# Optimization experiments

Measured on AMD Instinct MI355X. Metric: run time of the kernel, lower is better.

## Reference

```python
import jax, jax.numpy as jnp
import numpy as np

B, L, D, H = 8, 1024, 512, 8  # L must equal len_ for the skew trick
DH = D // H


def setup_inputs() -> dict:
    key = jax.random.key(0)
    ks = jax.random.split(key, 6)
    s = 0.02
    return {
        "x": jax.random.normal(ks[0], (B, L, D), dtype=jnp.float32),
        "Wq": jax.random.normal(ks[1], (D, D), dtype=jnp.float32) * s,
        "Wk": jax.random.normal(ks[2], (D, D), dtype=jnp.float32) * s,
        "Wv": jax.random.normal(ks[3], (D, D), dtype=jnp.float32) * s,
        "We": jax.random.normal(ks[4], (L, DH), dtype=jnp.float32) * s,  # e_projection weight: (len_, d_head)
        "Wo": jax.random.normal(ks[5], (D, D), dtype=jnp.float32) * s,
        "bo": jnp.zeros((D,), dtype=jnp.float32),
        "unused": 0,
    }


def reference(x, Wq, Wk, Wv, We, Wo, bo, unused):
    Bx, Lx, Dx = x.shape
    q = (x @ Wq.T).reshape(Bx, Lx, H, DH)  # blhd
    k = (x @ Wk.T).reshape(Bx, Lx, H, DH)
    v = (x @ Wv.T).reshape(Bx, Lx, H, DH)

    # relative-position logits: e_projection(q) then permute -> (B, H, L, len_)
    qe = jnp.einsum('blhd,ed->bhle', q, We)

    # 'skew' trick: reflect-pad right by L-1, zero-pad (right 1, bottom L-1),
    # reshape (B,H,2L-1,2L) -> (B,H,2L,2L-1), slice [:L, L-1:] -> (B,H,L,L)
    qe = jnp.pad(qe, ((0, 0), (0, 0), (0, 0), (0, Lx - 1)), mode='reflect')
    qe = jnp.pad(qe, ((0, 0), (0, 0), (0, Lx - 1), (0, 1)))
    qe = qe.reshape(Bx, H, 2 * Lx, 2 * Lx - 1)
    s_rel = qe[:, :, :Lx, Lx - 1:]

    scale = 1.0 / jnp.sqrt(jnp.asarray(DH, dtype=x.dtype))
    scores = jnp.einsum('blhd,bshd->bhls', q, k)
    A = jax.nn.softmax(scale * (scores + s_rel), axis=-1)
    V = jnp.einsum('bhls,bshd->blhd', A, v).reshape(Bx, Lx, Dx)
    return V @ Wo.T + bo
```

## Files before the change

### kernel.cpp

```cpp
#include <hip/hip_runtime.h>

#define Lc 1024
#define Dc 512
#define Hc 8
#define DHc 64

typedef __attribute__((ext_vector_type(8))) short bf16x8;
typedef __attribute__((ext_vector_type(4))) float f32x4;

typedef __attribute__((address_space(1))) const unsigned int guint;
typedef __attribute__((address_space(3))) unsigned int luint;

__device__ __forceinline__ void gload_lds16(const void* g, void* l) {
    __builtin_amdgcn_global_load_lds((guint*)g, (luint*)l, 16, 0, 0);
}

__device__ __forceinline__ unsigned short f2bf(float f) {
    unsigned u = __float_as_uint(f);
    u += 0x7fffu + ((u >> 16) & 1u);
    return (unsigned short)(u >> 16);
}
__device__ __forceinline__ unsigned short f2bft(float f) {
    return (unsigned short)(__float_as_uint(f) >> 16);
}
__device__ __forceinline__ unsigned pk2(float a, float b) {
    return (unsigned)f2bf(a) | ((unsigned)f2bf(b) << 16);
}
__device__ __forceinline__ float bf2f(unsigned short s) { return __uint_as_float(((unsigned)s) << 16); }

__global__ void cvt_all_kernel(
    const float* __restrict__ x,  const float* __restrict__ Wq,
    const float* __restrict__ Wk, const float* __restrict__ Wv,
    const float* __restrict__ Wo, const float* __restrict__ We,
    unsigned short* __restrict__ xb,  unsigned short* __restrict__ wqb,
    unsigned short* __restrict__ wkb, unsigned short* __restrict__ wvb,
    unsigned short* __restrict__ wob, unsigned short* __restrict__ wet)
{
    int bid = blockIdx.x;
    const float* src; unsigned short* dst; size_t base;
    if      (bid < 4096) { src = x;  dst = xb;  base = (size_t)bid * 1024; }
    else if (bid < 4352) { src = Wq; dst = wqb; base = (size_t)(bid-4096) * 1024; }
    else if (bid < 4608) { src = Wk; dst = wkb; base = (size_t)(bid-4352) * 1024; }
    else if (bid < 4864) { src = Wv; dst = wvb; base = (size_t)(bid-4608) * 1024; }
    else if (bid < 5120) { src = Wo; dst = wob; base = (size_t)(bid-4864) * 1024; }
    else                 { src = We; dst = wet; base = (size_t)(bid-5120) * 1024; }
    size_t i = base + (size_t)threadIdx.x * 4;
    float4 a = *(const float4*)&src[i];
    *(uint2*)&dst[i] = make_uint2(pk2(a.x, a.y), pk2(a.z, a.w));
}

__global__ __launch_bounds__(256, 3) void proj_mfma_kernel(
    const unsigned short* __restrict__ xb,
    const unsigned short* __restrict__ wq, const unsigned short* __restrict__ wk,
    const unsigned short* __restrict__ wv,
    unsigned short* __restrict__ qo, unsigned short* __restrict__ ko,
    unsigned short* __restrict__ vtg, float qscale)
{
    const unsigned short* W;
    if (blockIdx.z == 0)      W = wq;
    else if (blockIdx.z == 1) W = wk;
    else                      W = wv;

    __shared__ unsigned short smem[128 * 136];
    unsigned short* As = smem;
    unsigned short* Bs = smem + 8192;

    const int t = threadIdx.x;
    const int lane = t & 63, w = t >> 6;
    const int lq = lane >> 4, ln = lane & 15;
    const int m0 = blockIdx.y * 128, n0 = blockIdx.x * 128;
    const int wm = (w & 1) * 64, wn = (w >> 1) * 64;
    const int srow = t >> 3;
    const int lsg  = ((t & 7) ^ ((t >> 3) & 7)) * 8;
    const int key  = ln & 7;

    f32x4 acc[4][4];
    #pragma unroll
    for (int i = 0; i < 4; i++)
        #pragma unroll
        for (int j = 0; j < 4; j++) acc[i][j] = (f32x4){0.f,0.f,0.f,0.f};

    for (int c0 = 0; c0 < 512; c0 += 64) {
        __syncthreads();
        #pragma unroll
        for (int g = 0; g < 4; g++) {
            gload_lds16(&xb[(size_t)(m0 + 32*g + srow) * 512 + c0 + lsg], &As[(32*g + srow)*64 + (t&7)*8]);
            gload_lds16(&W [(size_t)(n0 + 32*g + srow) * 512 + c0 + lsg], &Bs[(32*g + srow)*64 + (t&7)*8]);
        }
        __syncthreads();

        #pragma unroll
        for (int kk = 0; kk < 2; kk++) {
            bf16x8 af[4], bf[4];
            #pragma unroll
            for (int i = 0; i < 4; i++)
                af[i] = *(bf16x8*)&As[(wm + 16*i + ln)*64 + ((kk*4 + lq) ^ key)*8];
            #pragma unroll
            for (int j = 0; j < 4; j++)
                bf[j] = *(bf16x8*)&Bs[(wn + 16*j + ln)*64 + ((kk*4 + lq) ^ key)*8];
            #pragma unroll
            for (int i = 0; i < 4; i++)
                #pragma unroll
                for (int j = 0; j < 4; j++)
                    acc[i][j] = __builtin_amdgcn_mfma_f32_16x16x32_bf16(af[i], bf[j], acc[i][j], 0, 0, 0);
        }
    }

    if (blockIdx.z < 2) {
        unsigned short* out = (blockIdx.z == 0) ? qo : ko;
        const float osc = (blockIdx.z == 0) ? qscale : 1.0f;
        #pragma unroll
        for (int i = 0; i < 4; i++) {
            #pragma unroll
            for (int r = 0; r < 4; r++) {
                int m = m0 + wm + 16*i + 4*lq + r;
                int b = m >> 10, l = m & 1023;
                #pragma unroll
                for (int j = 0; j < 4; j++) {
                    int n = n0 + wn + 16*j + ln;
                    int h = n >> 6, dh = n & 63;
                    out[((size_t)((b*Hc + h)*Lc + l))*DHc + dh] = f2bf(acc[i][j][r] * osc);
                }
            }
        }
    } else {
        __syncthreads();
        unsigned short* Ts = smem;
        #pragma unroll
        for (int i = 0; i < 4; i++) {
            int mlb = wm + 16*i + 4*lq;
            #pragma unroll
            for (int j = 0; j < 4; j++) {
                int nl = wn + 16*j + ln;
                *(uint2*)&Ts[nl*136 + mlb] = make_uint2(pk2(acc[i][j][0], acc[i][j][1]),
                                                        pk2(acc[i][j][2], acc[i][j][3]));
            }
        }
        __syncthreads();
        const int b = m0 >> 10, l0m = m0 & 1023;
        const int nl = t >> 1, seg = (t & 1) * 64;
        const int ng = n0 + nl, h = ng >> 6, dh = ng & 63;
        unsigned short* dst = vtg + (((size_t)(b*Hc + h))*DHc + dh)*Lc + l0m + seg;
        #pragma unroll
        for (int u = 0; u < 8; u++)
            *(uint4*)&dst[8*u] = *(uint4*)&Ts[nl*136 + seg + 8*u];
    }
}

__global__ __launch_bounds__(256, 4) void out_mfma_kernel(
    const unsigned short* __restrict__ A, const unsigned short* __restrict__ W,
    const float* __restrict__ bias, float* __restrict__ out)
{
    __shared__ unsigned short As[64 * 64];
    __shared__ unsigned short Bs[64 * 64];

    const int t = threadIdx.x;
    const int lane = t & 63, w = t >> 6;
    const int lq = lane >> 4, ln = lane & 15;
    const int m0 = blockIdx.y * 64, n0 = blockIdx.x * 64;
    const int wm = (w & 1) * 32, wn = (w >> 1) * 32;
    const int srow = t >> 3;
    const int lsg  = ((t & 7) ^ ((t >> 3) & 7)) * 8;
    const int key  = ln & 7;

    f32x4 acc[2][2];
    #pragma unroll
    for (int i = 0; i < 2; i++)
        #pragma unroll
        for (int j = 0; j < 2; j++) acc[i][j] = (f32x4){0.f,0.f,0.f,0.f};

    for (int c0 = 0; c0 < 512; c0 += 64) {
        __syncthreads();
        #pragma unroll
        for (int g = 0; g < 2; g++) {
            gload_lds16(&A[(size_t)(m0 + 32*g + srow) * 512 + c0 + lsg], &As[(32*g + srow)*64 + (t&7)*8]);
            gload_lds16(&W[(size_t)(n0 + 32*g + srow) * 512 + c0 + lsg], &Bs[(32*g + srow)*64 + (t&7)*8]);
        }
        __syncthreads();

        #pragma unroll
        for (int kk = 0; kk < 2; kk++) {
            bf16x8 af[2], bf[2];
            #pragma unroll
            for (int i = 0; i < 2; i++)
                af[i] = *(bf16x8*)&As[(wm + 16*i + ln)*64 + ((kk*4 + lq) ^ key)*8];
            #pragma unroll
            for (int j = 0; j < 2; j++)
                bf[j] = *(bf16x8*)&Bs[(wn + 16*j + ln)*64 + ((kk*4 + lq) ^ key)*8];
            #pragma unroll
            for (int i = 0; i < 2; i++)
                #pragma unroll
                for (int j = 0; j < 2; j++)
                    acc[i][j] = __builtin_amdgcn_mfma_f32_16x16x32_bf16(af[i], bf[j], acc[i][j], 0, 0, 0);
        }
    }

    float bb[2];
    #pragma unroll
    for (int j = 0; j < 2; j++) bb[j] = bias[n0 + wn + 16*j + ln];

    #pragma unroll
    for (int i = 0; i < 2; i++) {
        #pragma unroll
        for (int r = 0; r < 4; r++) {
            int m = m0 + wm + 16*i + 4*lq + r;
            #pragma unroll
            for (int j = 0; j < 2; j++) {
                int n = n0 + wn + 16*j + ln;
                out[(size_t)m * Dc + n] = acc[i][j][r] + bb[j];
            }
        }
    }
}

__global__ __launch_bounds__(256, 3) void attn_v5_kernel(
    const unsigned short* __restrict__ q, const unsigned short* __restrict__ k,
    const unsigned short* __restrict__ vtg, const unsigned short* __restrict__ wet,
    unsigned short* __restrict__ attn)
{
    __shared__ unsigned short ksp [2 * 64 * 32];
    __shared__ unsigned short vtp [2 * 64 * 32];
    __shared__ unsigned short wesp[2 * 64 * 32];
    __shared__ unsigned short ps  [2 * 64 * 32];
    __shared__ unsigned short qes [128 * 70];

    const int t    = threadIdx.x;
    const int lane = t & 63, w = t >> 6;
    const int lq   = lane >> 4, ln = lane & 15;

    const int n   = blockIdx.x;
    const int xcd = n & 7, idx = n >> 3;
    const int bh  = xcd * 8 + (idx >> 4);
    const int l0  = (idx & 15) * 64;

    const unsigned short* qb  = q   + (size_t)bh * (Lc * DHc);
    const unsigned short* kb  = k   + (size_t)bh * (Lc * DHc);
    const unsigned short* vtb = vtg + (size_t)bh * (DHc * Lc);

    const int trow = t >> 2;
    const int sseg = ((t & 3) ^ ((t >> 4) & 3)) * 8;
    const int swz  = (ln >> 2) & 3;

    const bf16x8 onesf = {(short)0x3F80,(short)0x3F80,(short)0x3F80,(short)0x3F80,
                          (short)0x3F80,(short)0x3F80,(short)0x3F80,(short)0x3F80};

    bf16x8 qa[2];
    #pragma unroll
    for (int kk = 0; kk < 2; kk++)
        qa[kk] = *(const bf16x8*)&qb[(size_t)(l0 + 16*w + ln)*64 + kk*32 + lq*8];

    const int pb0 = 15 - (l0 >> 6);
    gload_lds16(&wet[(size_t)(64*pb0 + trow)*64 +      sseg], &wesp[t*8]);
    gload_lds16(&wet[(size_t)(64*pb0 + trow)*64 + 32 + sseg], &wesp[2048 + t*8]);
    __syncthreads();
    {
        f32x4 qec[4];
        #pragma unroll
        for (int c = 0; c < 4; c++) qec[c] = (f32x4){0.f,0.f,0.f,0.f};
        #pragma unroll
        for (int kk = 0; kk < 2; kk++)
            #pragma unroll
            for (int c = 0; c < 4; c++) {
                bf16x8 bf = *(bf16x8*)&wesp[kk*2048 + (16*c + ln)*32 + (lq ^ swz)*8];
                qec[c] = __builtin_amdgcn_mfma_f32_16x16x32_bf16(qa[kk], bf, qec[c], 0, 0, 0);
            }
        const int cb = (pb0 & 1) * 64;
        #pragma unroll
        for (int c = 0; c < 4; c++)
            *(uint2*)&qes[(cb + 16*c + ln)*70 + 16*w + 4*lq] =
                make_uint2(pk2(qec[c][0], qec[c][1]), pk2(qec[c][2], qec[c][3]));
    }

    f32x4 Lacc = (f32x4){0.f, 0.f, 0.f, 0.f};
    f32x4 Ov[4];
    #pragma unroll
    for (int c = 0; c < 4; c++) Ov[c] = (f32x4){0.f, 0.f, 0.f, 0.f};

    int pbOld = pb0 - 1;

    for (int s0 = 0; s0 < Lc; s0 += 64) {
        const int c0  = l0 - s0;
        const int ac0 = c0 < 0 ? -c0 : c0;
        const int pb  = (960 - ac0) >> 6;
        const int newp = (pb > pbOld) ? pb + 1 : pb;
        pbOld = pb;
        const int cb = (newp & 1) * 64;

        __syncthreads();
        gload_lds16(&kb [(size_t)(s0 + trow)*64 +      sseg], &ksp [t*8]);
        gload_lds16(&kb [(size_t)(s0 + trow)*64 + 32 + sseg], &ksp [2048 + t*8]);
        gload_lds16(&vtb[(size_t)trow*1024 + s0 +      sseg], &vtp [t*8]);
        gload_lds16(&vtb[(size_t)trow*1024 + s0 + 32 + sseg], &vtp [2048 + t*8]);
        gload_lds16(&wet[(size_t)(64*newp + trow)*64 +      sseg], &wesp[t*8]);
        gload_lds16(&wet[(size_t)(64*newp + trow)*64 + 32 + sseg], &wesp[2048 + t*8]);
        __syncthreads();

        {
            f32x4 qec[4];
            #pragma unroll
            for (int c = 0; c < 4; c++) qec[c] = (f32x4){0.f,0.f,0.f,0.f};
            #pragma unroll
            for (int kk = 0; kk < 2; kk++)
                #pragma unroll
                for (int c = 0; c < 4; c++) {
                    bf16x8 bf = *(bf16x8*)&wesp[kk*2048 + (16*c + ln)*32 + (lq ^ swz)*8];
                    qec[c] = __builtin_amdgcn_mfma_f32_16x16x32_bf16(qa[kk], bf, qec[c], 0, 0, 0);
                }
            #pragma unroll
            for (int c = 0; c < 4; c++)
                *(uint2*)&qes[(cb + 16*c + ln)*70 + 16*w + 4*lq] =
                    make_uint2(pk2(qec[c][0], qec[c][1]), pk2(qec[c][2], qec[c][3]));
        }

        f32x4 sc[4];
        #pragma unroll
        for (int c = 0; c < 4; c++) sc[c] = (f32x4){0.f,0.f,0.f,0.f};
        #pragma unroll
        for (int kk = 0; kk < 2; kk++)
            #pragma unroll
            for (int c = 0; c < 4; c++) {
                bf16x8 bfk = *(bf16x8*)&ksp[kk*2048 + (16*c + ln)*32 + (lq ^ swz)*8];
                sc[c] = __builtin_amdgcn_mfma_f32_16x16x32_bf16(qa[kk], bfk, sc[c], 0, 0, 0);
            }

        float p[4][4];
        #pragma unroll
        for (int r = 0; r < 4; r++) {
            const int lr = 16*w + 4*lq + r;
            const int dbase = c0 + lr - ln;
            #pragma unroll
            for (int c = 0; c < 4; c++) {
                int d  = dbase - 16*c;
                int ad = d < 0 ? -d : d;
                int m  = 1023 - ad;
                float bias = bf2f(qes[(m & 127)*70 + lr]);
                p[r][c] = __builtin_amdgcn_exp2f(sc[c][r] + bias);
            }
        }

        #pragma unroll
        for (int r = 0; r < 4; r++) {
            const int lr = 16*w + 4*lq + r;
            #pragma unroll
            for (int c = 0; c < 4; c++) {
                int seg = (((c & 1)*2 + (ln >> 3)) ^ lq);
                ps[(c >> 1)*2048 + lr*32 + seg*8 + (ln & 7)] = f2bft(p[r][c]);
            }
        }

        #pragma unroll
        for (int kk = 0; kk < 2; kk++) {
            bf16x8 pa = *(bf16x8*)&ps[kk*2048 + (16*w + ln)*32 + (lq ^ swz)*8];
            Lacc = __builtin_amdgcn_mfma_f32_16x16x32_bf16(pa, onesf, Lacc, 0, 0, 0);
            #pragma unroll
            for (int c = 0; c < 4; c++) {
                bf16x8 vf = *(bf16x8*)&vtp[kk*2048 + (16*c + ln)*32 + (lq ^ swz)*8];
                Ov[c] = __builtin_amdgcn_mfma_f32_16x16x32_bf16(pa, vf, Ov[c], 0, 0, 0);
            }
        }
    }

    const int b = bh >> 3, h = bh & 7;
    #pragma unroll
    for (int r = 0; r < 4; r++) {
        float inv = 1.f / Lacc[r];
        int l = l0 + 16*w + 4*lq + r;
        #pragma unroll
        for (int c = 0; c < 4; c++)
            attn[((size_t)(b*Lc + l))*Dc + h*DHc + 16*c + ln] = f2bf(Ov[c][r] * inv);
    }
}

extern "C" void kernel_launch(void* const* d_in, const int* in_sizes, int n_in,
                              void* d_out, int out_size, void* d_ws, size_t ws_size,
                              hipStream_t stream)
{
    (void)in_sizes; (void)n_in; (void)out_size; (void)ws_size;
    const float* x  = (const float*)d_in[0];
    const float* Wq = (const float*)d_in[1];
    const float* Wk = (const float*)d_in[2];
    const float* Wv = (const float*)d_in[3];
    const float* We = (const float*)d_in[4];
    const float* Wo = (const float*)d_in[5];
    const float* bo = (const float*)d_in[6];

    const size_t NT = (size_t)8 * Hc * Lc * DHc;
    unsigned short* qw  = (unsigned short*)d_ws;
    unsigned short* kw  = qw  + NT;
    unsigned short* vtg = kw  + NT;
    unsigned short* xbf = vtg + NT;
    unsigned short* awb = xbf + NT;
    unsigned short* wqb = awb + NT;
    unsigned short* wkb = wqb + 262144;
    unsigned short* wvb = wkb + 262144;
    unsigned short* wob = wvb + 262144;
    unsigned short* wet = wob + 262144;

    cvt_all_kernel<<<5184, 256, 0, stream>>>(x, Wq, Wk, Wv, Wo, We,
                                             xbf, wqb, wkb, wvb, wob, wet);
    proj_mfma_kernel<<<dim3(4, 64, 3), 256, 0, stream>>>(xbf, wqb, wkb, wvb,
                                                         qw, kw, vtg,
                                                         0.125f * 1.44269504089f);
    attn_v5_kernel<<<1024, 256, 0, stream>>>(qw, kw, vtg, wet, awb);
    out_mfma_kernel<<<dim3(8, 128), 256, 0, stream>>>(awb, wob, bo, (float*)d_out);
}
```

Measured before the change: 180.5 us.

## Stage Q/K projection output through LDS and load We fragments directly to registers

The Q/K projection epilogue now writes bf16 results into shared memory first, then emits 16-byte coalesced stores into the head-major layout instead of scattered 2-byte stores. The attention kernel drops the LDS staging buffer for the relative-position weight tile. Each wave now loads its We MFMA fragments straight from global memory into registers, issued before the barrier so they overlap the K/V loads. This cuts LDS use and a barrier at the cost of more redundant global/L2 reads of We across waves and extra registers.

```diff
diff --git a/kernel.cpp b/kernel.cpp
--- a/kernel.cpp
+++ b/kernel.cpp
@@ -109,19 +109,25 @@
     if (blockIdx.z < 2) {
         unsigned short* out = (blockIdx.z == 0) ? qo : ko;
         const float osc = (blockIdx.z == 0) ? qscale : 1.0f;
-        #pragma unroll
-        for (int i = 0; i < 4; i++) {
+        __syncthreads();
+        unsigned short* Ts = smem;
+        #pragma unroll
+        for (int i = 0; i < 4; i++)
             #pragma unroll
             for (int r = 0; r < 4; r++) {
-                int m = m0 + wm + 16*i + 4*lq + r;
-                int b = m >> 10, l = m & 1023;
+                int ml = wm + 16*i + 4*lq + r;
                 #pragma unroll
-                for (int j = 0; j < 4; j++) {
-                    int n = n0 + wn + 16*j + ln;
-                    int h = n >> 6, dh = n & 63;
-                    out[((size_t)((b*Hc + h)*Lc + l))*DHc + dh] = f2bf(acc[i][j][r] * osc);
-                }
-            }
+                for (int j = 0; j < 4; j++)
+                    Ts[ml*136 + wn + 16*j + ln] = f2bf(acc[i][j][r] * osc);
+            }
+        __syncthreads();
+        const int rr = t >> 4, seg = t & 15;
+        #pragma unroll
+        for (int sw = 0; sw < 8; sw++) {
+            int ml = 16*sw + rr;
+            int m = m0 + ml, b = m >> 10, l = m & 1023;
+            int n = n0 + seg*8, h = n >> 6, dh = n & 63;
+            *(uint4*)&out[((size_t)((b*Hc + h)*Lc + l))*DHc + dh] = *(uint4*)&Ts[ml*136 + seg*8];
         }
     } else {
         __syncthreads();
@@ -213,14 +219,13 @@
     }
 }
 
-__global__ __launch_bounds__(256, 3) void attn_v5_kernel(
+__global__ __launch_bounds__(256, 3) void attn_v6_kernel(
     const unsigned short* __restrict__ q, const unsigned short* __restrict__ k,
     const unsigned short* __restrict__ vtg, const unsigned short* __restrict__ wet,
     unsigned short* __restrict__ attn)
 {
     __shared__ unsigned short ksp [2 * 64 * 32];
     __shared__ unsigned short vtp [2 * 64 * 32];
-    __shared__ unsigned short wesp[2 * 64 * 32];
     __shared__ unsigned short ps  [2 * 64 * 32];
     __shared__ unsigned short qes [128 * 70];
 
@@ -250,9 +255,6 @@
         qa[kk] = *(const bf16x8*)&qb[(size_t)(l0 + 16*w + ln)*64 + kk*32 + lq*8];
 
     const int pb0 = 15 - (l0 >> 6);
-    gload_lds16(&wet[(size_t)(64*pb0 + trow)*64 +      sseg], &wesp[t*8]);
-    gload_lds16(&wet[(size_t)(64*pb0 + trow)*64 + 32 + sseg], &wesp[2048 + t*8]);
-    __syncthreads();
     {
         f32x4 qec[4];
         #pragma unroll
@@ -261,7 +263,7 @@
         for (int kk = 0; kk < 2; kk++)
             #pragma unroll
             for (int c = 0; c < 4; c++) {
-                bf16x8 bf = *(bf16x8*)&wesp[kk*2048 + (16*c + ln)*32 + (lq ^ swz)*8];
+                bf16x8 bf = *(const bf16x8*)&wet[(size_t)(64*pb0 + 16*c + ln)*64 + kk*32 + lq*8];
                 qec[c] = __builtin_amdgcn_mfma_f32_16x16x32_bf16(qa[kk], bf, qec[c], 0, 0, 0);
             }
         const int cb = (pb0 & 1) * 64;
@@ -286,13 +288,18 @@
         pbOld = pb;
         const int cb = (newp & 1) * 64;
 
+        bf16x8 wef[2][4];
+        #pragma unroll
+        for (int kk = 0; kk < 2; kk++)
+            #pragma unroll
+            for (int c = 0; c < 4; c++)
+                wef[kk][c] = *(const bf16x8*)&wet[(size_t)(64*newp + 16*c + ln)*64 + kk*32 + lq*8];
+
         __syncthreads();
         gload_lds16(&kb [(size_t)(s0 + trow)*64 +      sseg], &ksp [t*8]);
         gload_lds16(&kb [(size_t)(s0 + trow)*64 + 32 + sseg], &ksp [2048 + t*8]);
         gload_lds16(&vtb[(size_t)trow*1024 + s0 +      sseg], &vtp [t*8]);
         gload_lds16(&vtb[(size_t)trow*1024 + s0 + 32 + sseg], &vtp [2048 + t*8]);
-        gload_lds16(&wet[(size_t)(64*newp + trow)*64 +      sseg], &wesp[t*8]);
-        gload_lds16(&wet[(size_t)(64*newp + trow)*64 + 32 + sseg], &wesp[2048 + t*8]);
         __syncthreads();
 
         {
@@ -302,10 +309,8 @@
             #pragma unroll
             for (int kk = 0; kk < 2; kk++)
                 #pragma unroll
-                for (int c = 0; c < 4; c++) {
-                    bf16x8 bf = *(bf16x8*)&wesp[kk*2048 + (16*c + ln)*32 + (lq ^ swz)*8];
-                    qec[c] = __builtin_amdgcn_mfma_f32_16x16x32_bf16(qa[kk], bf, qec[c], 0, 0, 0);
-                }
+                for (int c = 0; c < 4; c++)
+                    qec[c] = __builtin_amdgcn_mfma_f32_16x16x32_bf16(qa[kk], wef[kk][c], qec[c], 0, 0, 0);
             #pragma unroll
             for (int c = 0; c < 4; c++)
                 *(uint2*)&qes[(cb + 16*c + ln)*70 + 16*w + 4*lq] =
@@ -401,6 +406,6 @@
     proj_mfma_kernel<<<dim3(4, 64, 3), 256, 0, stream>>>(xbf, wqb, wkb, wvb,
                                                          qw, kw, vtg,
                                                          0.125f * 1.44269504089f);
-    attn_v5_kernel<<<1024, 256, 0, stream>>>(qw, kw, vtg, wet, awb);
+    attn_v6_kernel<<<1024, 256, 0, stream>>>(qw, kw, vtg, wet, awb);
     out_mfma_kernel<<<dim3(8, 128), 256, 0, stream>>>(awb, wob, bo, (float*)d_out);
 }
```

New measurement: 207.8 us. 15.1% more time.
